# Performance work log

Measured on AMD Instinct MI355X. Metric: run time of the kernel, lower is better.

The kernel has to match this reference:

```python
import jax, jax.numpy as jnp
import numpy as np

B, L, D_MODEL, D_STATE, D_HIDDEN = 4, 4096, 1024, 256, 4096
RMIN, RMAX, MAX_PHASE = 0.8, 0.95, 2.0 * np.pi


def setup_inputs() -> dict:
    key = jax.random.key(0)
    ks = jax.random.split(key, 10)
    # LRU ring init (Orvieto et al.): |lambda| in [rmin, rmax], phase in [0, max_phase)
    u1 = jax.random.uniform(ks[0], (D_STATE,))
    u2 = jax.random.uniform(ks[1], (D_STATE,))
    nu_log = jnp.log(-0.5 * jnp.log(u1 * (RMAX**2 - RMIN**2) + RMIN**2))
    theta_log = jnp.log(MAX_PHASE * u2)
    B_re = jax.random.normal(ks[2], (D_STATE, D_MODEL)) / np.sqrt(2.0 * D_MODEL)
    B_im = jax.random.normal(ks[3], (D_STATE, D_MODEL)) / np.sqrt(2.0 * D_MODEL)
    C_re = jax.random.normal(ks[4], (D_MODEL, D_STATE)) / np.sqrt(D_STATE)
    C_im = jax.random.normal(ks[5], (D_MODEL, D_STATE)) / np.sqrt(D_STATE)
    D_mat = jax.random.normal(ks[6], (D_MODEL, D_MODEL)) / np.sqrt(D_MODEL)
    W1 = jax.random.normal(ks[7], (D_MODEL, D_HIDDEN)) * np.sqrt(2.0 / D_MODEL)
    W2 = jax.random.normal(ks[8], (D_HIDDEN, D_MODEL)) * np.sqrt(2.0 / D_HIDDEN)
    res_logit = jnp.asarray(-1.0, dtype=jnp.float32)
    x3d = jax.random.normal(ks[9], (B, L, D_MODEL), dtype=jnp.float32)
    return {"x3d": x3d, "nu_log": nu_log, "theta_log": theta_log,
            "B_re": B_re, "B_im": B_im, "C_re": C_re, "C_im": C_im,
            "D_mat": D_mat, "W1": W1, "W2": W2, "res_logit": res_logit}


def _lru_scan(lam, Bu):
    # diagonal linear recurrence x_t = lam * x_{t-1} + Bu_t via associative scan
    lam_b = jnp.broadcast_to(lam, Bu.shape)  # [B, L, N]

    def comb(a, b):
        return (a[0] * b[0], b[0] * a[1] + b[1])

    _, states = jax.lax.associative_scan(comb, (lam_b, Bu), axis=1)
    return states  # [B, L, N] complex


def reference(x3d, nu_log, theta_log, B_re, B_im, C_re, C_im, D_mat, W1, W2, res_logit):
    lam = jnp.exp(-jnp.exp(nu_log) + 1j * jnp.exp(theta_log))          # [N]
    gamma = jnp.sqrt(1.0 - jnp.abs(lam) ** 2)                           # [N]
    Bn = (gamma[:, None] * (B_re + 1j * B_im))                          # [N, D]
    Bu = jnp.einsum('bld,nd->bln', x3d.astype(jnp.complex64), Bn)       # [B, L, N]
    states = _lru_scan(lam.astype(jnp.complex64), Bu)                   # [B, L, N]
    y = jnp.einsum('bln,mn->blm', states, C_re + 1j * C_im).real \
        + jnp.einsum('bld,md->blm', x3d, D_mat)                         # [B, L, D]
    # MLP feedforward (nl_layers=2, bias=False), dropout is identity at p=0
    z = jax.nn.gelu(y @ W1) @ W2                                        # [B, L, D]
    out = x3d + jax.nn.sigmoid(res_logit) * z
    st = states[:, -1]  # final recurrent state
    return out, st
```

## Files before the change

### kernel.cpp

```cpp
#include <hip/hip_runtime.h>
#include <stdint.h>

typedef __bf16 bf16;
typedef bf16 bf16x8 __attribute__((ext_vector_type(8)));
typedef float f32x4 __attribute__((ext_vector_type(4)));

#define B_  4
#define L_  4096
#define DM  1024
#define DS  256
#define DH  4096
#define BL  16384
#define CL  64
#define NC  64

__device__ __forceinline__ float bfbits(uint32_t lo16) {
  union { uint32_t u; float f; } v; v.u = lo16 << 16; return v.f;
}

__device__ __forceinline__ void async16(const bf16* g, bf16* l) {
  __builtin_amdgcn_global_load_lds(
      (const __attribute__((address_space(1))) uint32_t*)g,
      (__attribute__((address_space(3))) uint32_t*)l, 16, 0, 0);
}

#define SYNC_PRE()  do { asm volatile("" ::: "memory"); __builtin_amdgcn_s_barrier(); } while (0)
#define SYNC_POST() do { __builtin_amdgcn_s_barrier(); asm volatile("" ::: "memory"); } while (0)
#define LGKM0()     asm volatile("s_waitcnt lgkmcnt(0)" ::: "memory")

__global__ void phaseA(const float* __restrict__ nu_log,
                       const float* __restrict__ th_log,
                       float* __restrict__ scal) {
  int n = threadIdx.x;
  float nu = __expf(nu_log[n]);
  float th = __expf(th_log[n]);
  float mod = __expf(-nu);
  float lr = mod * cosf(th);
  float li = mod * sinf(th);
  float g = sqrtf(fmaxf(1.0f - mod * mod, 0.0f));
  float pr = 1.f, pi = 0.f;
  for (int i = 0; i < CL; i++) {
    float nr = pr * lr - pi * li;
    float ni = pr * li + pi * lr;
    pr = nr; pi = ni;
  }
  scal[n] = lr; scal[256 + n] = li;
  scal[512 + n] = pr; scal[768 + n] = pi;
  scal[1024 + n] = g;
}

__global__ void prep_bu(const float* __restrict__ B_re, const float* __restrict__ B_im,
                        const float* __restrict__ scal, bf16* __restrict__ WB) {
  size_t i = (size_t)blockIdx.x * 256 + threadIdx.x;
  int row = (int)(i >> 10), col = (int)(i & 1023);
  int n = row >> 1;
  const float* src = (row & 1) ? B_im : B_re;
  WB[i] = (bf16)(scal[1024 + n] * src[n * 1024 + col]);
}

__global__ void prep_y(const float* __restrict__ C_re, const float* __restrict__ C_im,
                       const float* __restrict__ D_mat, bf16* __restrict__ WB) {
  size_t i = (size_t)blockIdx.x * 256 + threadIdx.x;
  int m = (int)(i / 1536), c = (int)(i % 1536);
  float v;
  if (c < 256)       v = C_re[m * 256 + c];
  else if (c < 512)  v = -C_im[m * 256 + (c - 256)];
  else               v = D_mat[m * 1024 + (c - 512)];
  WB[i] = (bf16)v;
}

__global__ void transpose_to_bf16(const float* __restrict__ in, bf16* __restrict__ out,
                                  int R, int C) {
  __shared__ float tile[32][33];
  int c0 = blockIdx.x * 32, r0 = blockIdx.y * 32;
  int tx = threadIdx.x, ty = threadIdx.y;
  for (int i = 0; i < 32; i += 8)
    tile[ty + i][tx] = in[(size_t)(r0 + ty + i) * C + c0 + tx];
  __syncthreads();
  for (int i = 0; i < 32; i += 8)
    out[(size_t)(c0 + ty + i) * R + r0 + tx] = (bf16)tile[tx][ty + i];
}

__global__ void conv_x(const float4* __restrict__ x, bf16* __restrict__ XS) {
  size_t i = (size_t)blockIdx.x * 256 + threadIdx.x;
  size_t t = i >> 8;
  int d4 = (int)(i & 255);
  float4 v = x[i];
  bf16* o = XS + t * 1536 + 512 + (size_t)d4 * 4;
  o[0] = (bf16)v.x; o[1] = (bf16)v.y; o[2] = (bf16)v.z; o[3] = (bf16)v.w;
}

template <int EPI>
__device__ __forceinline__ void epi_store(void* C, int ldc, size_t row, size_t col,
                                          float v, float sig, const float* xres) {
  size_t off = row * (size_t)ldc + col;
  if (EPI == 0) {
    ((bf16*)C)[off] = (bf16)v;
  } else if (EPI == 1) {
    float z = 0.7978845608f * (v + 0.044715f * v * v * v);
    float gv = v / (1.f + __expf(-2.f * z));
    ((bf16*)C)[off] = (bf16)gv;
  } else {
    ((float*)C)[off] = xres[off] + sig * v;
  }
}

template <int EPI>
__global__ __launch_bounds__(512, 2) void gemm256(
    const bf16* __restrict__ A, int lda,
    const bf16* __restrict__ Bt, int ldb,
    void* __restrict__ C, int ldc, int NK, int mt, int nt,
    const float* __restrict__ xres, const float* __restrict__ reslog) {
  __shared__ __align__(16) bf16 sA[2 * 2 * 8192];
  __shared__ __align__(16) bf16 sB[2 * 2 * 8192];

  const int tid  = threadIdx.x;
  const int lane = tid & 63;
  const int wave = tid >> 6;
  const int q = lane >> 4, l16 = lane & 15;
  const int wr = wave >> 2, wc = wave & 3;

  int nb = mt * nt;
  int per = nb >> 3;
  int t0 = (blockIdx.x & 7) * per + (blockIdx.x >> 3);
  int gsz = nt << 3;
  int g = t0 / gsz, r = t0 % gsz;
  size_t m0 = (size_t)(g * 8 + (r & 7)) * 256;
  size_t n0 = (size_t)(r >> 3) * 256;

  const int srow = tid >> 3;
  const int scol = ((tid & 7) << 3) ^ ((srow & 12) << 2);
  const bf16* gA = A  + (m0 + srow) * (size_t)lda + scol;
  const bf16* gB = Bt + (n0 + srow) * (size_t)ldb + scol;
  bf16* lA = sA + tid * 8;
  bf16* lB = sB + tid * 8;

  auto stageA = [&](int kt, int w) {
    const bf16* s = gA + (size_t)(w * 128) * lda + kt * 64;
    bf16* l = lA + ((kt & 1) * 16384 + w * 8192);
    async16(s, l);
    async16(s + (size_t)64 * lda, l + 4096);
  };
  auto stageB = [&](int kt, int w) {
    const bf16* s = gB + (size_t)(w * 128) * ldb + kt * 64;
    bf16* l = lB + ((kt & 1) * 16384 + w * 8192);
    async16(s, l);
    async16(s + (size_t)64 * ldb, l + 4096);
  };

  stageA(0, 0); stageA(0, 1); stageB(0, 0); stageB(0, 1);
  stageB(1, 0); stageB(1, 1);
  __builtin_amdgcn_s_waitcnt(0x0F74);
  __builtin_amdgcn_s_barrier();
  asm volatile("" ::: "memory");

  const int sw  = (l16 & 12) << 2;
  const int qx0 = (q << 3) ^ sw;
  const int qx1 = ((q << 3) + 32) ^ sw;
  const bf16* Ard = sA + wr * 8192 + l16 * 64;
  const bf16* Brd = sB + (wc >> 1) * 8192 + ((wc & 1) * 64 + l16) * 64;

  f32x4 acc[8][4] = {};
  bf16x8 a[4][2], b[4][2];

  for (int t = 0; t < NK; ++t) {
    const int d = (t & 1) * 16384;
    const bf16* Ab = Ard + d;
    const bf16* Bb = Brd + d;

#pragma unroll
    for (int j = 0; j < 4; ++j) a[j][0] = *(const bf16x8*)&Ab[j * 1024 + qx0];
#pragma unroll
    for (int n = 0; n < 4; ++n) b[n][0] = *(const bf16x8*)&Bb[n * 1024 + qx0];
    if (t + 1 < NK) stageA(t + 1, 0);
    SYNC_PRE(); LGKM0();
    __builtin_amdgcn_s_setprio(1);
#pragma unroll
    for (int j = 0; j < 4; ++j)
#pragma unroll
      for (int n = 0; n < 4; ++n)
        acc[j][n] = __builtin_amdgcn_mfma_f32_16x16x32_bf16(a[j][0], b[n][0], acc[j][n], 0, 0, 0);
    __builtin_amdgcn_s_setprio(0);
    SYNC_POST();

#pragma unroll
    for (int j = 0; j < 4; ++j) a[j][1] = *(const bf16x8*)&Ab[j * 1024 + qx1];
#pragma unroll
    for (int n = 0; n < 4; ++n) b[n][1] = *(const bf16x8*)&Bb[n * 1024 + qx1];
    if (t + 1 < NK) stageA(t + 1, 1);
    SYNC_PRE(); LGKM0();
    __builtin_amdgcn_s_setprio(1);
#pragma unroll
    for (int j = 0; j < 4; ++j)
#pragma unroll
      for (int n = 0; n < 4; ++n)
        acc[j][n] = __builtin_amdgcn_mfma_f32_16x16x32_bf16(a[j][1], b[n][1], acc[j][n], 0, 0, 0);
    __builtin_amdgcn_s_setprio(0);
    SYNC_POST();

#pragma unroll
    for (int j = 0; j < 4; ++j) a[j][0] = *(const bf16x8*)&Ab[(4 + j) * 1024 + qx0];
    if (t + 2 < NK) stageB(t + 2, 0);
    SYNC_PRE(); LGKM0();
    __builtin_amdgcn_s_setprio(1);
#pragma unroll
    for (int j = 0; j < 4; ++j)
#pragma unroll
      for (int n = 0; n < 4; ++n)
        acc[4 + j][n] = __builtin_amdgcn_mfma_f32_16x16x32_bf16(a[j][0], b[n][0], acc[4 + j][n], 0, 0, 0);
    __builtin_amdgcn_s_setprio(0);
    SYNC_POST();

#pragma unroll
    for (int j = 0; j < 4; ++j) a[j][1] = *(const bf16x8*)&Ab[(4 + j) * 1024 + qx1];
    if (t + 2 < NK) {
      stageB(t + 2, 1);
      __builtin_amdgcn_s_waitcnt(0x0F74);
    } else if (t + 1 < NK) {
      __builtin_amdgcn_s_waitcnt(0x0F70);
    }
    SYNC_PRE(); LGKM0();
    __builtin_amdgcn_s_setprio(1);
#pragma unroll
    for (int j = 0; j < 4; ++j)
#pragma unroll
      for (int n = 0; n < 4; ++n)
        acc[4 + j][n] = __builtin_amdgcn_mfma_f32_16x16x32_bf16(a[j][1], b[n][1], acc[4 + j][n], 0, 0, 0);
    __builtin_amdgcn_s_setprio(0);
    SYNC_POST();
  }

  float sig = 0.f;
  if (EPI == 2) sig = 1.f / (1.f + __expf(-reslog[0]));
#pragma unroll
  for (int mi = 0; mi < 8; ++mi)
#pragma unroll
    for (int ni = 0; ni < 4; ++ni) {
      size_t col = n0 + wc * 64 + ni * 16 + l16;
#pragma unroll
      for (int r2 = 0; r2 < 4; ++r2) {
        size_t row = m0 + wr * 128 + mi * 16 + q * 4 + r2;
        epi_store<EPI>(C, ldc, row, col, acc[mi][ni][r2], sig, xres);
      }
    }
}

template <int EPI>
__global__ __launch_bounds__(512, 2) void gemm128(
    const bf16* __restrict__ A, int lda,
    const bf16* __restrict__ Bt, int ldb,
    void* __restrict__ C, int ldc, int NK, int mt, int nt,
    const float* __restrict__ xres, const float* __restrict__ reslog) {
  __shared__ __align__(16) bf16 sA[2 * 8192];
  __shared__ __align__(16) bf16 sB[3 * 16384];

  const int tid  = threadIdx.x;
  const int lane = tid & 63;
  const int wave = tid >> 6;
  const int q = lane >> 4, l16 = lane & 15;
  const int wr = wave >> 2, wc = wave & 3;

  int nb = mt * nt;
  int per = nb >> 3;
  int t0 = (blockIdx.x & 7) * per + (blockIdx.x >> 3);
  int gsz = nt << 3;
  int g = t0 / gsz, r = t0 % gsz;
  size_t m0 = (size_t)(g * 8 + (r & 7)) * 128;
  size_t n0 = (size_t)(r >> 3) * 256;

  const int srow = tid >> 3;
  const int scol = ((tid & 7) << 3) ^ ((srow & 12) << 2);
  const bf16* gA = A  + (m0 + srow) * (size_t)lda + scol;
  const bf16* gB = Bt + (n0 + srow) * (size_t)ldb + scol;
  bf16* lA = sA + tid * 8;
  bf16* lB = sB + tid * 8;

  auto stageA = [&](int kt) {
    const bf16* s = gA + kt * 64;
    bf16* l = lA + (kt & 1) * 8192;
    async16(s, l);
    async16(s + (size_t)64 * lda, l + 4096);
  };
  auto stageB = [&](int kt, int w) {
    const bf16* s = gB + (size_t)(w * 128) * ldb + kt * 64;
    bf16* l = lB + ((kt % 3) * 16384 + w * 8192);
    async16(s, l);
    async16(s + (size_t)64 * ldb, l + 4096);
  };

  stageA(0); stageB(0, 0); stageB(0, 1);
  stageB(1, 0); stageB(1, 1);
  __builtin_amdgcn_s_waitcnt(0x0F74);
  __builtin_amdgcn_s_barrier();
  asm volatile("" ::: "memory");

  const int sw  = (l16 & 12) << 2;
  const int qx0 = (q << 3) ^ sw;
  const int qx1 = ((q << 3) + 32) ^ sw;
  const bf16* Ard = sA + (wr * 64 + l16) * 64;
  const bf16* Brd = sB + (wc >> 1) * 8192 + ((wc & 1) * 64 + l16) * 64;

  f32x4 acc[4][4] = {};
  bf16x8 a[4][2], b[4][2];

  for (int t = 0; t < NK; ++t) {
    const bf16* Ab = Ard + (t & 1) * 8192;
    const bf16* Bb = Brd + (t % 3) * 16384;

#pragma unroll
    for (int j = 0; j < 4; ++j) a[j][0] = *(const bf16x8*)&Ab[j * 1024 + qx0];
#pragma unroll
    for (int n = 0; n < 4; ++n) b[n][0] = *(const bf16x8*)&Bb[n * 1024 + qx0];
    if (t + 1 < NK) stageA(t + 1);
    SYNC_PRE(); LGKM0();
    __builtin_amdgcn_s_setprio(1);
#pragma unroll
    for (int j = 0; j < 4; ++j)
#pragma unroll
      for (int n = 0; n < 4; ++n)
        acc[j][n] = __builtin_amdgcn_mfma_f32_16x16x32_bf16(a[j][0], b[n][0], acc[j][n], 0, 0, 0);
    __builtin_amdgcn_s_setprio(0);
    SYNC_POST();

#pragma unroll
    for (int j = 0; j < 4; ++j) a[j][1] = *(const bf16x8*)&Ab[j * 1024 + qx1];
#pragma unroll
    for (int n = 0; n < 4; ++n) b[n][1] = *(const bf16x8*)&Bb[n * 1024 + qx1];
    if (t + 2 < NK) {
      stageB(t + 2, 0); stageB(t + 2, 1);
      __builtin_amdgcn_s_waitcnt(0x0F74);
    } else if (t + 1 < NK) {
      __builtin_amdgcn_s_waitcnt(0x0F70);
    }
    SYNC_PRE(); LGKM0();
    __builtin_amdgcn_s_setprio(1);
#pragma unroll
    for (int j = 0; j < 4; ++j)
#pragma unroll
      for (int n = 0; n < 4; ++n)
        acc[j][n] = __builtin_amdgcn_mfma_f32_16x16x32_bf16(a[j][1], b[n][1], acc[j][n], 0, 0, 0);
    __builtin_amdgcn_s_setprio(0);
    SYNC_POST();
  }

  float sig = 0.f;
  if (EPI == 2) sig = 1.f / (1.f + __expf(-reslog[0]));
#pragma unroll
  for (int mi = 0; mi < 4; ++mi)
#pragma unroll
    for (int ni = 0; ni < 4; ++ni) {
      size_t col = n0 + wc * 64 + ni * 16 + l16;
#pragma unroll
      for (int r2 = 0; r2 < 4; ++r2) {
        size_t row = m0 + wr * 64 + mi * 16 + q * 4 + r2;
        epi_store<EPI>(C, ldc, row, col, acc[mi][ni][r2], sig, xres);
      }
    }
}

__global__ void scan_pass1(const bf16* __restrict__ Bu, const float* __restrict__ scal,
                           float2* __restrict__ H) {
  int b = blockIdx.x >> 6, c = blockIdx.x & 63, n = threadIdx.x;
  float lr = scal[n], li = scal[256 + n];
  float sr = 0.f, si = 0.f;
  size_t t0 = (size_t)b * L_ + (size_t)c * CL;
  const uint32_t* p = (const uint32_t*)(Bu + t0 * 512) + n;
  for (int j = 0; j < CL; j++) {
    uint32_t u = p[(size_t)j * 256];
    float ur = bfbits(u & 0xffffu), ui = bfbits(u >> 16);
    float nr = lr * sr - li * si + ur;
    float ni = lr * si + li * sr + ui;
    sr = nr; si = ni;
  }
  H[(size_t)(b * NC + c) * 256 + n] = make_float2(sr, si);
}

__global__ void scan_pass2(const float2* __restrict__ H, const float* __restrict__ scal,
                           float2* __restrict__ Carry) {
  int b = blockIdx.x, n = threadIdx.x;
  float Pr = scal[512 + n], Pi = scal[768 + n];
  float cr = 0.f, ci = 0.f;
  for (int c = 0; c < NC; c++) {
    Carry[(size_t)(b * NC + c) * 256 + n] = make_float2(cr, ci);
    float2 h = H[(size_t)(b * NC + c) * 256 + n];
    float nr = Pr * cr - Pi * ci + h.x;
    float ni = Pr * ci + Pi * cr + h.y;
    cr = nr; ci = ni;
  }
}

__global__ void scan_pass3(const bf16* __restrict__ Bu, const float* __restrict__ scal,
                           const float2* __restrict__ Carry, bf16* __restrict__ XS,
                           float* __restrict__ st) {
  int b = blockIdx.x >> 6, c = blockIdx.x & 63, n = threadIdx.x;
  float lr = scal[n], li = scal[256 + n];
  float2 cv = Carry[(size_t)(b * NC + c) * 256 + n];
  float sr = cv.x, si = cv.y;
  size_t t0 = (size_t)b * L_ + (size_t)c * CL;
  const uint32_t* p = (const uint32_t*)(Bu + t0 * 512) + n;
  bf16* qp = XS + t0 * 1536 + n;
  for (int j = 0; j < CL; j++) {
    uint32_t u = p[(size_t)j * 256];
    float ur = bfbits(u & 0xffffu), ui = bfbits(u >> 16);
    float nr = lr * sr - li * si + ur;
    float ni = lr * si + li * sr + ui;
    sr = nr; si = ni;
    qp[(size_t)j * 1536] = (bf16)sr;
    qp[(size_t)j * 1536 + 256] = (bf16)si;
  }
  if (c == NC - 1) {
    st[(size_t)b * 256 + n] = sr;
    st[1024 + (size_t)b * 256 + n] = si;
  }
}

extern "C" void kernel_launch(void* const* d_in, const int* in_sizes, int n_in,
                              void* d_out, int out_size, void* d_ws, size_t ws_size,
                              hipStream_t stream) {
  const float* x      = (const float*)d_in[0];
  const float* nu_log = (const float*)d_in[1];
  const float* th_log = (const float*)d_in[2];
  const float* B_re   = (const float*)d_in[3];
  const float* B_im   = (const float*)d_in[4];
  const float* C_re   = (const float*)d_in[5];
  const float* C_im   = (const float*)d_in[6];
  const float* D_mat  = (const float*)d_in[7];
  const float* W1     = (const float*)d_in[8];
  const float* W2     = (const float*)d_in[9];
  const float* reslog = (const float*)d_in[10];

  char* wsb = (char*)d_ws;
  size_t off = 0;
  auto alloc = [&](size_t bytes) {
    void* p = wsb + off;
    off += (bytes + 255) & ~(size_t)255;
    return p;
  };
  float*  scal = (float*)alloc(5 * 256 * 4);
  bf16*   WBbu = (bf16*)alloc((size_t)512 * 1024 * 2);
  bf16*   WBy  = (bf16*)alloc((size_t)1024 * 1536 * 2);
  bf16*   WB1  = (bf16*)alloc((size_t)4096 * 1024 * 2);
  bf16*   WB2  = (bf16*)alloc((size_t)1024 * 4096 * 2);
  float2* H    = (float2*)alloc((size_t)B_ * NC * 256 * 8);
  float2* Cr   = (float2*)alloc((size_t)B_ * NC * 256 * 8);
  bf16*   Ybf  = (bf16*)alloc((size_t)BL * 1024 * 2);
  bf16*   XS   = (bf16*)alloc((size_t)BL * 1536 * 2);
  bf16*   Bu   = (bf16*)alloc((size_t)BL * 512 * 2);
  bf16*   Hbf  = XS;

  float* out = (float*)d_out;
  float* st  = out + (size_t)BL * DM;

  phaseA<<<1, 256, 0, stream>>>(nu_log, th_log, scal);
  prep_bu<<<512 * 1024 / 256, 256, 0, stream>>>(B_re, B_im, scal, WBbu);
  prep_y<<<1024 * 1536 / 256, 256, 0, stream>>>(C_re, C_im, D_mat, WBy);
  transpose_to_bf16<<<dim3(4096 / 32, 1024 / 32), dim3(32, 8), 0, stream>>>(W1, WB1, 1024, 4096);
  transpose_to_bf16<<<dim3(1024 / 32, 4096 / 32), dim3(32, 8), 0, stream>>>(W2, WB2, 4096, 1024);
  conv_x<<<BL * 256 / 256, 256, 0, stream>>>((const float4*)x, XS);

  gemm128<0><<<128 * 2, 512, 0, stream>>>(
      XS + 512, 1536, WBbu, 1024, Bu, 512, 16, 128, 2, nullptr, nullptr);

  scan_pass1<<<B_ * NC, 256, 0, stream>>>(Bu, scal, H);
  scan_pass2<<<B_, 256, 0, stream>>>(H, scal, Cr);
  scan_pass3<<<B_ * NC, 256, 0, stream>>>(Bu, scal, Cr, XS, st);

  gemm256<0><<<64 * 4, 512, 0, stream>>>(
      XS, 1536, WBy, 1536, Ybf, 1024, 24, 64, 4, nullptr, nullptr);

  for (int i = 0; i < 2; i++) {
    const bf16* Yc = Ybf + (size_t)i * 8192 * 1024;
    float* Oc = out + (size_t)i * 8192 * 1024;
    const float* Xc = x + (size_t)i * 8192 * 1024;
    gemm256<1><<<32 * 16, 512, 0, stream>>>(
        Yc, 1024, WB1, 1024, Hbf, 4096, 16, 32, 16, nullptr, nullptr);
    gemm128<2><<<64 * 4, 512, 0, stream>>>(
        Hbf, 4096, WB2, 4096, Oc, 1024, 64, 64, 4, Xc, reslog);
  }
}
```

Baseline: 610.7 us.

## Simplify GEMM pipeline to one barrier per k-tile with full-tile staging

Both GEMM kernels drop the four-phase (gemm256) and two-phase (gemm128) interleaved loops, which used a barrier pair per phase, in favour of a plain double buffer. Each iteration now loads all LDS fragments up front, issues the full next-tile async loads, runs all MFMAs, then waits and barriers once. The LDS swizzle changes to an XOR over 8-row groups, and gemm128's triple-buffered B shrinks to two buffers. Far fewer barriers should cut sync overhead, but prefetch distance drops to one tile and register pressure rises, so memory latency may be less hidden.

```diff
diff --git a/kernel.cpp b/kernel.cpp
--- a/kernel.cpp
+++ b/kernel.cpp
@@ -24,9 +24,7 @@
       (__attribute__((address_space(3))) uint32_t*)l, 16, 0, 0);
 }
 
-#define SYNC_PRE()  do { asm volatile("" ::: "memory"); __builtin_amdgcn_s_barrier(); } while (0)
-#define SYNC_POST() do { __builtin_amdgcn_s_barrier(); asm volatile("" ::: "memory"); } while (0)
-#define LGKM0()     asm volatile("s_waitcnt lgkmcnt(0)" ::: "memory")
+#define MEMFENCE() asm volatile("" ::: "memory")
 
 __global__ void phaseA(const float* __restrict__ nu_log,
                        const float* __restrict__ th_log,
@@ -111,8 +109,8 @@
     const bf16* __restrict__ Bt, int ldb,
     void* __restrict__ C, int ldc, int NK, int mt, int nt,
     const float* __restrict__ xres, const float* __restrict__ reslog) {
-  __shared__ __align__(16) bf16 sA[2 * 2 * 8192];
-  __shared__ __align__(16) bf16 sB[2 * 2 * 8192];
+  __shared__ __align__(16) bf16 sA[2 * 16384];
+  __shared__ __align__(16) bf16 sB[2 * 16384];
 
   const int tid  = threadIdx.x;
   const int lane = tid & 63;
@@ -129,39 +127,42 @@
   size_t n0 = (size_t)(r >> 3) * 256;
 
   const int srow = tid >> 3;
-  const int scol = ((tid & 7) << 3) ^ ((srow & 12) << 2);
+  const int scol = (((tid & 7) ^ ((tid >> 3) & 7)) << 3);
   const bf16* gA = A  + (m0 + srow) * (size_t)lda + scol;
   const bf16* gB = Bt + (n0 + srow) * (size_t)ldb + scol;
   bf16* lA = sA + tid * 8;
   bf16* lB = sB + tid * 8;
 
-  auto stageA = [&](int kt, int w) {
-    const bf16* s = gA + (size_t)(w * 128) * lda + kt * 64;
-    bf16* l = lA + ((kt & 1) * 16384 + w * 8192);
+  auto stageA = [&](int kt) {
+    const bf16* s = gA + kt * 64;
+    bf16* l = lA + (kt & 1) * 16384;
     async16(s, l);
-    async16(s + (size_t)64 * lda, l + 4096);
+    async16(s + (size_t)64  * lda, l + 4096);
+    async16(s + (size_t)128 * lda, l + 8192);
+    async16(s + (size_t)192 * lda, l + 12288);
   };
-  auto stageB = [&](int kt, int w) {
-    const bf16* s = gB + (size_t)(w * 128) * ldb + kt * 64;
-    bf16* l = lB + ((kt & 1) * 16384 + w * 8192);
+  auto stageB = [&](int kt) {
+    const bf16* s = gB + kt * 64;
+    bf16* l = lB + (kt & 1) * 16384;
     async16(s, l);
-    async16(s + (size_t)64 * ldb, l + 4096);
+    async16(s + (size_t)64  * ldb, l + 4096);
+    async16(s + (size_t)128 * ldb, l + 8192);
+    async16(s + (size_t)192 * ldb, l + 12288);
   };
 
-  stageA(0, 0); stageA(0, 1); stageB(0, 0); stageB(0, 1);
-  stageB(1, 0); stageB(1, 1);
-  __builtin_amdgcn_s_waitcnt(0x0F74);
+  stageA(0); stageB(0);
+  __builtin_amdgcn_s_waitcnt(0x0F70);
   __builtin_amdgcn_s_barrier();
-  asm volatile("" ::: "memory");
-
-  const int sw  = (l16 & 12) << 2;
+  MEMFENCE();
+
+  const int sw  = (l16 & 7) << 3;
   const int qx0 = (q << 3) ^ sw;
   const int qx1 = ((q << 3) + 32) ^ sw;
   const bf16* Ard = sA + wr * 8192 + l16 * 64;
   const bf16* Brd = sB + (wc >> 1) * 8192 + ((wc & 1) * 64 + l16) * 64;
 
   f32x4 acc[8][4] = {};
-  bf16x8 a[4][2], b[4][2];
+  bf16x8 aL[4][2], aH[4][2], b[4][2];
 
   for (int t = 0; t < NK; ++t) {
     const int d = (t & 1) * 16384;
@@ -169,65 +170,51 @@
     const bf16* Bb = Brd + d;
 
 #pragma unroll
-    for (int j = 0; j < 4; ++j) a[j][0] = *(const bf16x8*)&Ab[j * 1024 + qx0];
-#pragma unroll
-    for (int n = 0; n < 4; ++n) b[n][0] = *(const bf16x8*)&Bb[n * 1024 + qx0];
-    if (t + 1 < NK) stageA(t + 1, 0);
-    SYNC_PRE(); LGKM0();
+    for (int j = 0; j < 4; ++j) {
+      aL[j][0] = *(const bf16x8*)&Ab[j * 1024 + qx0];
+      aL[j][1] = *(const bf16x8*)&Ab[j * 1024 + qx1];
+    }
+#pragma unroll
+    for (int n = 0; n < 4; ++n) {
+      b[n][0] = *(const bf16x8*)&Bb[n * 1024 + qx0];
+      b[n][1] = *(const bf16x8*)&Bb[n * 1024 + qx1];
+    }
+    if (t + 1 < NK) { stageA(t + 1); stageB(t + 1); }
+    MEMFENCE();
+
     __builtin_amdgcn_s_setprio(1);
 #pragma unroll
     for (int j = 0; j < 4; ++j)
 #pragma unroll
       for (int n = 0; n < 4; ++n)
-        acc[j][n] = __builtin_amdgcn_mfma_f32_16x16x32_bf16(a[j][0], b[n][0], acc[j][n], 0, 0, 0);
+        acc[j][n] = __builtin_amdgcn_mfma_f32_16x16x32_bf16(aL[j][0], b[n][0], acc[j][n], 0, 0, 0);
+#pragma unroll
+    for (int j = 0; j < 4; ++j)
+#pragma unroll
+      for (int n = 0; n < 4; ++n)
+        acc[j][n] = __builtin_amdgcn_mfma_f32_16x16x32_bf16(aL[j][1], b[n][1], acc[j][n], 0, 0, 0);
+
+#pragma unroll
+    for (int j = 0; j < 4; ++j) {
+      aH[j][0] = *(const bf16x8*)&Ab[(4 + j) * 1024 + qx0];
+      aH[j][1] = *(const bf16x8*)&Ab[(4 + j) * 1024 + qx1];
+    }
+#pragma unroll
+    for (int j = 0; j < 4; ++j)
+#pragma unroll
+      for (int n = 0; n < 4; ++n)
+        acc[4 + j][n] = __builtin_amdgcn_mfma_f32_16x16x32_bf16(aH[j][0], b[n][0], acc[4 + j][n], 0, 0, 0);
+#pragma unroll
+    for (int j = 0; j < 4; ++j)
+#pragma unroll
+      for (int n = 0; n < 4; ++n)
+        acc[4 + j][n] = __builtin_amdgcn_mfma_f32_16x16x32_bf16(aH[j][1], b[n][1], acc[4 + j][n], 0, 0, 0);
     __builtin_amdgcn_s_setprio(0);
-    SYNC_POST();
-
-#pragma unroll
-    for (int j = 0; j < 4; ++j) a[j][1] = *(const bf16x8*)&Ab[j * 1024 + qx1];
-#pragma unroll
-    for (int n = 0; n < 4; ++n) b[n][1] = *(const bf16x8*)&Bb[n * 1024 + qx1];
-    if (t + 1 < NK) stageA(t + 1, 1);
-    SYNC_PRE(); LGKM0();
-    __builtin_amdgcn_s_setprio(1);
-#pragma unroll
-    for (int j = 0; j < 4; ++j)
-#pragma unroll
-      for (int n = 0; n < 4; ++n)
-        acc[j][n] = __builtin_amdgcn_mfma_f32_16x16x32_bf16(a[j][1], b[n][1], acc[j][n], 0, 0, 0);
-    __builtin_amdgcn_s_setprio(0);
-    SYNC_POST();
-
-#pragma unroll
-    for (int j = 0; j < 4; ++j) a[j][0] = *(const bf16x8*)&Ab[(4 + j) * 1024 + qx0];
-    if (t + 2 < NK) stageB(t + 2, 0);
-    SYNC_PRE(); LGKM0();
-    __builtin_amdgcn_s_setprio(1);
-#pragma unroll
-    for (int j = 0; j < 4; ++j)
-#pragma unroll
-      for (int n = 0; n < 4; ++n)
-        acc[4 + j][n] = __builtin_amdgcn_mfma_f32_16x16x32_bf16(a[j][0], b[n][0], acc[4 + j][n], 0, 0, 0);
-    __builtin_amdgcn_s_setprio(0);
-    SYNC_POST();
-
-#pragma unroll
-    for (int j = 0; j < 4; ++j) a[j][1] = *(const bf16x8*)&Ab[(4 + j) * 1024 + qx1];
-    if (t + 2 < NK) {
-      stageB(t + 2, 1);
-      __builtin_amdgcn_s_waitcnt(0x0F74);
-    } else if (t + 1 < NK) {
-      __builtin_amdgcn_s_waitcnt(0x0F70);
-    }
-    SYNC_PRE(); LGKM0();
-    __builtin_amdgcn_s_setprio(1);
-#pragma unroll
-    for (int j = 0; j < 4; ++j)
-#pragma unroll
-      for (int n = 0; n < 4; ++n)
-        acc[4 + j][n] = __builtin_amdgcn_mfma_f32_16x16x32_bf16(a[j][1], b[n][1], acc[4 + j][n], 0, 0, 0);
-    __builtin_amdgcn_s_setprio(0);
-    SYNC_POST();
+
+    MEMFENCE();
+    __builtin_amdgcn_s_waitcnt(0x0F70);
+    __builtin_amdgcn_s_barrier();
+    MEMFENCE();
   }
 
   float sig = 0.f;
@@ -252,7 +239,7 @@
     void* __restrict__ C, int ldc, int NK, int mt, int nt,
     const float* __restrict__ xres, const float* __restrict__ reslog) {
   __shared__ __align__(16) bf16 sA[2 * 8192];
-  __shared__ __align__(16) bf16 sB[3 * 16384];
+  __shared__ __align__(16) bf16 sB[2 * 16384];
 
   const int tid  = threadIdx.x;
   const int lane = tid & 63;
@@ -269,7 +256,7 @@
   size_t n0 = (size_t)(r >> 3) * 256;
 
   const int srow = tid >> 3;
-  const int scol = ((tid & 7) << 3) ^ ((srow & 12) << 2);
+  const int scol = (((tid & 7) ^ ((tid >> 3) & 7)) << 3);
   const bf16* gA = A  + (m0 + srow) * (size_t)lda + scol;
   const bf16* gB = Bt + (n0 + srow) * (size_t)ldb + scol;
   bf16* lA = sA + tid * 8;
@@ -281,20 +268,21 @@
     async16(s, l);
     async16(s + (size_t)64 * lda, l + 4096);
   };
-  auto stageB = [&](int kt, int w) {
-    const bf16* s = gB + (size_t)(w * 128) * ldb + kt * 64;
-    bf16* l = lB + ((kt % 3) * 16384 + w * 8192);
+  auto stageB = [&](int kt) {
+    const bf16* s = gB + kt * 64;
+    bf16* l = lB + (kt & 1) * 16384;
     async16(s, l);
-    async16(s + (size_t)64 * ldb, l + 4096);
+    async16(s + (size_t)64  * ldb, l + 4096);
+    async16(s + (size_t)128 * ldb, l + 8192);
+    async16(s + (size_t)192 * ldb, l + 12288);
   };
 
-  stageA(0); stageB(0, 0); stageB(0, 1);
-  stageB(1, 0); stageB(1, 1);
-  __builtin_amdgcn_s_waitcnt(0x0F74);
+  stageA(0); stageB(0);
+  __builtin_amdgcn_s_waitcnt(0x0F70);
   __builtin_amdgcn_s_barrier();
-  asm volatile("" ::: "memory");
-
-  const int sw  = (l16 & 12) << 2;
+  MEMFENCE();
+
+  const int sw  = (l16 & 7) << 3;
   const int qx0 = (q << 3) ^ sw;
   const int qx1 = ((q << 3) + 32) ^ sw;
   const bf16* Ard = sA + (wr * 64 + l16) * 64;
@@ -305,42 +293,38 @@
 
   for (int t = 0; t < NK; ++t) {
     const bf16* Ab = Ard + (t & 1) * 8192;
-    const bf16* Bb = Brd + (t % 3) * 16384;
-
-#pragma unroll
-    for (int j = 0; j < 4; ++j) a[j][0] = *(const bf16x8*)&Ab[j * 1024 + qx0];
-#pragma unroll
-    for (int n = 0; n < 4; ++n) b[n][0] = *(const bf16x8*)&Bb[n * 1024 + qx0];
-    if (t + 1 < NK) stageA(t + 1);
-    SYNC_PRE(); LGKM0();
+    const bf16* Bb = Brd + (t & 1) * 16384;
+
+#pragma unroll
+    for (int j = 0; j < 4; ++j) {
+      a[j][0] = *(const bf16x8*)&Ab[j * 1024 + qx0];
+      a[j][1] = *(const bf16x8*)&Ab[j * 1024 + qx1];
+    }
+#pragma unroll
+    for (int n = 0; n < 4; ++n) {
+      b[n][0] = *(const bf16x8*)&Bb[n * 1024 + qx0];
+      b[n][1] = *(const bf16x8*)&Bb[n * 1024 + qx1];
+    }
+    if (t + 1 < NK) { stageA(t + 1); stageB(t + 1); }
+    MEMFENCE();
+
     __builtin_amdgcn_s_setprio(1);
 #pragma unroll
     for (int j = 0; j < 4; ++j)
 #pragma unroll
       for (int n = 0; n < 4; ++n)
         acc[j][n] = __builtin_amdgcn_mfma_f32_16x16x32_bf16(a[j][0], b[n][0], acc[j][n], 0, 0, 0);
-    __builtin_amdgcn_s_setprio(0);
-    SYNC_POST();
-
-#pragma unroll
-    for (int j = 0; j < 4; ++j) a[j][1] = *(const bf16x8*)&Ab[j * 1024 + qx1];
-#pragma unroll
-    for (int n = 0; n < 4; ++n) b[n][1] = *(const bf16x8*)&Bb[n * 1024 + qx1];
-    if (t + 2 < NK) {
-      stageB(t + 2, 0); stageB(t + 2, 1);
-      __builtin_amdgcn_s_waitcnt(0x0F74);
-    } else if (t + 1 < NK) {
-      __builtin_amdgcn_s_waitcnt(0x0F70);
-    }
-    SYNC_PRE(); LGKM0();
-    __builtin_amdgcn_s_setprio(1);
 #pragma unroll
     for (int j = 0; j < 4; ++j)
 #pragma unroll
       for (int n = 0; n < 4; ++n)
         acc[j][n] = __builtin_amdgcn_mfma_f32_16x16x32_bf16(a[j][1], b[n][1], acc[j][n], 0, 0, 0);
     __builtin_amdgcn_s_setprio(0);
-    SYNC_POST();
+
+    MEMFENCE();
+    __builtin_amdgcn_s_waitcnt(0x0F70);
+    __builtin_amdgcn_s_barrier();
+    MEMFENCE();
   }
 
   float sig = 0.f;
```

New measurement: 569.7 us. 1.07x faster.

## Restructure GEMM LDS pipeline: full-K fragment loads, 3-stage A buffer, new swizzle

Applied to the files above, without the earlier changes.

Both bf16 GEMM kernels now load both K-halves of the A/B fragments together and split each phase by N-halves instead of K-halves. gemm128 gets a triple-buffered A tile with rotating buffer indices and prefetches A and B two tiles ahead. The LDS swizzle changes to an XOR on the low three row bits to cut bank conflicts. The aim is to overlap global-to-LDS copies with MFMA work and reduce LDS stalls. The cost is more LDS per block, more live registers, and one LGKM wait removed before the last phase of gemm256, which needs care for correctness.

```diff
diff --git a/kernel.cpp b/kernel.cpp
--- a/kernel.cpp
+++ b/kernel.cpp
@@ -24,8 +24,9 @@
       (__attribute__((address_space(3))) uint32_t*)l, 16, 0, 0);
 }
 
-#define SYNC_PRE()  do { asm volatile("" ::: "memory"); __builtin_amdgcn_s_barrier(); } while (0)
-#define SYNC_POST() do { __builtin_amdgcn_s_barrier(); asm volatile("" ::: "memory"); } while (0)
+#define MEMFENCE()  asm volatile("" ::: "memory")
+#define SYNC_PRE()  do { MEMFENCE(); __builtin_amdgcn_s_barrier(); } while (0)
+#define SYNC_POST() do { __builtin_amdgcn_s_barrier(); MEMFENCE(); } while (0)
 #define LGKM0()     asm volatile("s_waitcnt lgkmcnt(0)" ::: "memory")
 
 __global__ void phaseA(const float* __restrict__ nu_log,
@@ -111,8 +112,8 @@
     const bf16* __restrict__ Bt, int ldb,
     void* __restrict__ C, int ldc, int NK, int mt, int nt,
     const float* __restrict__ xres, const float* __restrict__ reslog) {
-  __shared__ __align__(16) bf16 sA[2 * 2 * 8192];
-  __shared__ __align__(16) bf16 sB[2 * 2 * 8192];
+  __shared__ __align__(16) bf16 sA[2 * 16384];
+  __shared__ __align__(16) bf16 sB[2 * 16384];
 
   const int tid  = threadIdx.x;
   const int lane = tid & 63;
@@ -129,32 +130,34 @@
   size_t n0 = (size_t)(r >> 3) * 256;
 
   const int srow = tid >> 3;
-  const int scol = ((tid & 7) << 3) ^ ((srow & 12) << 2);
+  const int scol = (((tid & 7) ^ ((tid >> 3) & 7)) << 3);
   const bf16* gA = A  + (m0 + srow) * (size_t)lda + scol;
   const bf16* gB = Bt + (n0 + srow) * (size_t)ldb + scol;
   bf16* lA = sA + tid * 8;
   bf16* lB = sB + tid * 8;
 
-  auto stageA = [&](int kt, int w) {
-    const bf16* s = gA + (size_t)(w * 128) * lda + kt * 64;
-    bf16* l = lA + ((kt & 1) * 16384 + w * 8192);
+  auto stageA = [&](int kt) {
+    const bf16* s = gA + kt * 64;
+    bf16* l = lA + (kt & 1) * 16384;
     async16(s, l);
-    async16(s + (size_t)64 * lda, l + 4096);
+    async16(s + (size_t)64  * lda, l + 4096);
+    async16(s + (size_t)128 * lda, l + 8192);
+    async16(s + (size_t)192 * lda, l + 12288);
   };
-  auto stageB = [&](int kt, int w) {
-    const bf16* s = gB + (size_t)(w * 128) * ldb + kt * 64;
-    bf16* l = lB + ((kt & 1) * 16384 + w * 8192);
+  auto stageB = [&](int kt, int h) {
+    const bf16* s = gB + (size_t)(h * 128) * ldb + kt * 64;
+    bf16* l = lB + (kt & 1) * 16384 + h * 8192;
     async16(s, l);
     async16(s + (size_t)64 * ldb, l + 4096);
   };
 
-  stageA(0, 0); stageA(0, 1); stageB(0, 0); stageB(0, 1);
+  stageA(0); stageB(0, 0); stageB(0, 1);
   stageB(1, 0); stageB(1, 1);
   __builtin_amdgcn_s_waitcnt(0x0F74);
   __builtin_amdgcn_s_barrier();
-  asm volatile("" ::: "memory");
-
-  const int sw  = (l16 & 12) << 2;
+  MEMFENCE();
+
+  const int sw  = (l16 & 7) << 3;
   const int qx0 = (q << 3) ^ sw;
   const int qx1 = ((q << 3) + 32) ^ sw;
   const bf16* Ard = sA + wr * 8192 + l16 * 64;
@@ -163,69 +166,84 @@
   f32x4 acc[8][4] = {};
   bf16x8 a[4][2], b[4][2];
 
-  for (int t = 0; t < NK; ++t) {
-    const int d = (t & 1) * 16384;
+  for (int kt = 0; kt < NK; ++kt) {
+    const int d = (kt & 1) * 16384;
     const bf16* Ab = Ard + d;
     const bf16* Bb = Brd + d;
 
 #pragma unroll
-    for (int j = 0; j < 4; ++j) a[j][0] = *(const bf16x8*)&Ab[j * 1024 + qx0];
-#pragma unroll
-    for (int n = 0; n < 4; ++n) b[n][0] = *(const bf16x8*)&Bb[n * 1024 + qx0];
-    if (t + 1 < NK) stageA(t + 1, 0);
+    for (int j = 0; j < 4; ++j) {
+      a[j][0] = *(const bf16x8*)&Ab[j * 1024 + qx0];
+      a[j][1] = *(const bf16x8*)&Ab[j * 1024 + qx1];
+    }
+#pragma unroll
+    for (int n = 0; n < 2; ++n) {
+      b[n][0] = *(const bf16x8*)&Bb[n * 1024 + qx0];
+      b[n][1] = *(const bf16x8*)&Bb[n * 1024 + qx1];
+    }
+    if (kt + 1 < NK) stageA(kt + 1);
     SYNC_PRE(); LGKM0();
     __builtin_amdgcn_s_setprio(1);
 #pragma unroll
     for (int j = 0; j < 4; ++j)
 #pragma unroll
-      for (int n = 0; n < 4; ++n)
+      for (int n = 0; n < 2; ++n) {
         acc[j][n] = __builtin_amdgcn_mfma_f32_16x16x32_bf16(a[j][0], b[n][0], acc[j][n], 0, 0, 0);
+        acc[j][n] = __builtin_amdgcn_mfma_f32_16x16x32_bf16(a[j][1], b[n][1], acc[j][n], 0, 0, 0);
+      }
     __builtin_amdgcn_s_setprio(0);
     SYNC_POST();
 
 #pragma unroll
-    for (int j = 0; j < 4; ++j) a[j][1] = *(const bf16x8*)&Ab[j * 1024 + qx1];
-#pragma unroll
-    for (int n = 0; n < 4; ++n) b[n][1] = *(const bf16x8*)&Bb[n * 1024 + qx1];
-    if (t + 1 < NK) stageA(t + 1, 1);
+    for (int n = 2; n < 4; ++n) {
+      b[n][0] = *(const bf16x8*)&Bb[n * 1024 + qx0];
+      b[n][1] = *(const bf16x8*)&Bb[n * 1024 + qx1];
+    }
     SYNC_PRE(); LGKM0();
     __builtin_amdgcn_s_setprio(1);
 #pragma unroll
     for (int j = 0; j < 4; ++j)
 #pragma unroll
-      for (int n = 0; n < 4; ++n)
+      for (int n = 2; n < 4; ++n) {
+        acc[j][n] = __builtin_amdgcn_mfma_f32_16x16x32_bf16(a[j][0], b[n][0], acc[j][n], 0, 0, 0);
         acc[j][n] = __builtin_amdgcn_mfma_f32_16x16x32_bf16(a[j][1], b[n][1], acc[j][n], 0, 0, 0);
+      }
     __builtin_amdgcn_s_setprio(0);
     SYNC_POST();
 
 #pragma unroll
-    for (int j = 0; j < 4; ++j) a[j][0] = *(const bf16x8*)&Ab[(4 + j) * 1024 + qx0];
-    if (t + 2 < NK) stageB(t + 2, 0);
+    for (int j = 0; j < 4; ++j) {
+      a[j][0] = *(const bf16x8*)&Ab[(4 + j) * 1024 + qx0];
+      a[j][1] = *(const bf16x8*)&Ab[(4 + j) * 1024 + qx1];
+    }
+    if (kt + 2 < NK) stageB(kt + 2, 0);
     SYNC_PRE(); LGKM0();
     __builtin_amdgcn_s_setprio(1);
 #pragma unroll
     for (int j = 0; j < 4; ++j)
 #pragma unroll
-      for (int n = 0; n < 4; ++n)
+      for (int n = 0; n < 2; ++n) {
         acc[4 + j][n] = __builtin_amdgcn_mfma_f32_16x16x32_bf16(a[j][0], b[n][0], acc[4 + j][n], 0, 0, 0);
+        acc[4 + j][n] = __builtin_amdgcn_mfma_f32_16x16x32_bf16(a[j][1], b[n][1], acc[4 + j][n], 0, 0, 0);
+      }
     __builtin_amdgcn_s_setprio(0);
     SYNC_POST();
 
-#pragma unroll
-    for (int j = 0; j < 4; ++j) a[j][1] = *(const bf16x8*)&Ab[(4 + j) * 1024 + qx1];
-    if (t + 2 < NK) {
-      stageB(t + 2, 1);
+    if (kt + 2 < NK) {
+      stageB(kt + 2, 1);
       __builtin_amdgcn_s_waitcnt(0x0F74);
-    } else if (t + 1 < NK) {
+    } else if (kt + 1 < NK) {
       __builtin_amdgcn_s_waitcnt(0x0F70);
     }
-    SYNC_PRE(); LGKM0();
+    SYNC_PRE();
     __builtin_amdgcn_s_setprio(1);
 #pragma unroll
     for (int j = 0; j < 4; ++j)
 #pragma unroll
-      for (int n = 0; n < 4; ++n)
+      for (int n = 2; n < 4; ++n) {
+        acc[4 + j][n] = __builtin_amdgcn_mfma_f32_16x16x32_bf16(a[j][0], b[n][0], acc[4 + j][n], 0, 0, 0);
         acc[4 + j][n] = __builtin_amdgcn_mfma_f32_16x16x32_bf16(a[j][1], b[n][1], acc[4 + j][n], 0, 0, 0);
+      }
     __builtin_amdgcn_s_setprio(0);
     SYNC_POST();
   }
@@ -251,7 +269,7 @@
     const bf16* __restrict__ Bt, int ldb,
     void* __restrict__ C, int ldc, int NK, int mt, int nt,
     const float* __restrict__ xres, const float* __restrict__ reslog) {
-  __shared__ __align__(16) bf16 sA[2 * 8192];
+  __shared__ __align__(16) bf16 sA[3 * 8192];
   __shared__ __align__(16) bf16 sB[3 * 16384];
 
   const int tid  = threadIdx.x;
@@ -269,32 +287,32 @@
   size_t n0 = (size_t)(r >> 3) * 256;
 
   const int srow = tid >> 3;
-  const int scol = ((tid & 7) << 3) ^ ((srow & 12) << 2);
+  const int scol = (((tid & 7) ^ ((tid >> 3) & 7)) << 3);
   const bf16* gA = A  + (m0 + srow) * (size_t)lda + scol;
   const bf16* gB = Bt + (n0 + srow) * (size_t)ldb + scol;
   bf16* lA = sA + tid * 8;
   bf16* lB = sB + tid * 8;
 
-  auto stageA = [&](int kt) {
+  auto stageA = [&](int kt, int buf) {
     const bf16* s = gA + kt * 64;
-    bf16* l = lA + (kt & 1) * 8192;
+    bf16* l = lA + buf * 8192;
     async16(s, l);
     async16(s + (size_t)64 * lda, l + 4096);
   };
-  auto stageB = [&](int kt, int w) {
-    const bf16* s = gB + (size_t)(w * 128) * ldb + kt * 64;
-    bf16* l = lB + ((kt % 3) * 16384 + w * 8192);
+  auto stageB = [&](int kt, int buf, int h) {
+    const bf16* s = gB + (size_t)(h * 128) * ldb + kt * 64;
+    bf16* l = lB + buf * 16384 + h * 8192;
     async16(s, l);
     async16(s + (size_t)64 * ldb, l + 4096);
   };
 
-  stageA(0); stageB(0, 0); stageB(0, 1);
-  stageB(1, 0); stageB(1, 1);
-  __builtin_amdgcn_s_waitcnt(0x0F74);
+  stageB(0, 0, 0); stageB(0, 0, 1); stageA(0, 0);
+  stageB(1, 1, 0); stageB(1, 1, 1); stageA(1, 1);
+  __builtin_amdgcn_s_waitcnt(0x0F76);
   __builtin_amdgcn_s_barrier();
-  asm volatile("" ::: "memory");
-
-  const int sw  = (l16 & 12) << 2;
+  MEMFENCE();
+
+  const int sw  = (l16 & 7) << 3;
   const int qx0 = (q << 3) ^ sw;
   const int qx1 = ((q << 3) + 32) ^ sw;
   const bf16* Ard = sA + (wr * 64 + l16) * 64;
@@ -303,33 +321,43 @@
   f32x4 acc[4][4] = {};
   bf16x8 a[4][2], b[4][2];
 
-  for (int t = 0; t < NK; ++t) {
-    const bf16* Ab = Ard + (t & 1) * 8192;
-    const bf16* Bb = Brd + (t % 3) * 16384;
-
-#pragma unroll
-    for (int j = 0; j < 4; ++j) a[j][0] = *(const bf16x8*)&Ab[j * 1024 + qx0];
-#pragma unroll
-    for (int n = 0; n < 4; ++n) b[n][0] = *(const bf16x8*)&Bb[n * 1024 + qx0];
-    if (t + 1 < NK) stageA(t + 1);
+  int c0 = 0, c2 = 2;
+  for (int kt = 0; kt < NK; ++kt) {
+    const bf16* Ab = Ard + c0 * 8192;
+    const bf16* Bb = Brd + c0 * 16384;
+
+#pragma unroll
+    for (int j = 0; j < 4; ++j) {
+      a[j][0] = *(const bf16x8*)&Ab[j * 1024 + qx0];
+      a[j][1] = *(const bf16x8*)&Ab[j * 1024 + qx1];
+    }
+#pragma unroll
+    for (int n = 0; n < 2; ++n) {
+      b[n][0] = *(const bf16x8*)&Bb[n * 1024 + qx0];
+      b[n][1] = *(const bf16x8*)&Bb[n * 1024 + qx1];
+    }
+    if (kt + 2 < NK) { stageB(kt + 2, c2, 0); stageB(kt + 2, c2, 1); }
     SYNC_PRE(); LGKM0();
     __builtin_amdgcn_s_setprio(1);
 #pragma unroll
     for (int j = 0; j < 4; ++j)
 #pragma unroll
-      for (int n = 0; n < 4; ++n)
+      for (int n = 0; n < 2; ++n) {
         acc[j][n] = __builtin_amdgcn_mfma_f32_16x16x32_bf16(a[j][0], b[n][0], acc[j][n], 0, 0, 0);
+        acc[j][n] = __builtin_amdgcn_mfma_f32_16x16x32_bf16(a[j][1], b[n][1], acc[j][n], 0, 0, 0);
+      }
     __builtin_amdgcn_s_setprio(0);
     SYNC_POST();
 
 #pragma unroll
-    for (int j = 0; j < 4; ++j) a[j][1] = *(const bf16x8*)&Ab[j * 1024 + qx1];
-#pragma unroll
-    for (int n = 0; n < 4; ++n) b[n][1] = *(const bf16x8*)&Bb[n * 1024 + qx1];
-    if (t + 2 < NK) {
-      stageB(t + 2, 0); stageB(t + 2, 1);
-      __builtin_amdgcn_s_waitcnt(0x0F74);
-    } else if (t + 1 < NK) {
+    for (int n = 2; n < 4; ++n) {
+      b[n][0] = *(const bf16x8*)&Bb[n * 1024 + qx0];
+      b[n][1] = *(const bf16x8*)&Bb[n * 1024 + qx1];
+    }
+    if (kt + 2 < NK) {
+      stageA(kt + 2, c2);
+      __builtin_amdgcn_s_waitcnt(0x0F76);
+    } else if (kt + 1 < NK) {
       __builtin_amdgcn_s_waitcnt(0x0F70);
     }
     SYNC_PRE(); LGKM0();
@@ -337,10 +365,15 @@
 #pragma unroll
     for (int j = 0; j < 4; ++j)
 #pragma unroll
-      for (int n = 0; n < 4; ++n)
+      for (int n = 2; n < 4; ++n) {
+        acc[j][n] = __builtin_amdgcn_mfma_f32_16x16x32_bf16(a[j][0], b[n][0], acc[j][n], 0, 0, 0);
         acc[j][n] = __builtin_amdgcn_mfma_f32_16x16x32_bf16(a[j][1], b[n][1], acc[j][n], 0, 0, 0);
+      }
     __builtin_amdgcn_s_setprio(0);
     SYNC_POST();
+
+    c0 = (c0 == 2) ? 0 : c0 + 1;
+    c2 = (c2 == 2) ? 0 : c2 + 1;
   }
 
   float sig = 0.f;
```

Result: faster. 561.7 us (-8.0%).
